# Optimization experiments

Hardware: AMD Instinct MI355X
Metric: run time of the kernel (lower is better)

## Reference

```python
import jax, jax.numpy as jnp
import numpy as np


def setup_inputs() -> dict:
    key = jax.random.key(0)
    k0, k1, k2, k3 = jax.random.split(key, 4)
    T, H, I, E = 2048, 2048, 5632, 8
    return {
        "hidden_states": jax.random.normal(k0, (T, H), dtype=jnp.float32),
        "gate_w": jax.random.normal(k1, (E, H), dtype=jnp.float32) * 0.02,
        "w1": jax.random.normal(k2, (E, 2 * I, H), dtype=jnp.float32) * 0.02,
        "w2": jax.random.normal(k3, (E, H, I), dtype=jnp.float32) * 0.02,
        "top_k": 2,
    }


def reference(hidden_states, gate_w, w1, w2, top_k):
    # hidden_states: [T, H]; gate_w: [E, H]; w1: [E, 2I, H]; w2: [E, H, I]
    T = hidden_states.shape[0]
    E = w1.shape[0]
    router_logits = hidden_states @ gate_w.T                    # [T, E]
    probs = jax.nn.softmax(router_logits, axis=-1)
    topk_w, topk_idx = jax.lax.top_k(probs, top_k)              # [T, k]
    # renormalize=False in fused_moe: use raw softmax top-k weights.
    # Dense combine matrix C[t, e] = weight of expert e for token t (0 if unrouted).
    combine = jnp.zeros((T, E), dtype=probs.dtype)
    combine = combine.at[jnp.arange(T)[:, None], topk_idx].add(topk_w)
    out = jnp.zeros_like(hidden_states)
    for e in range(E):  # small fixed expert loop
        gate_up = hidden_states @ w1[e].T                       # [T, 2I]
        g, u = jnp.split(gate_up, 2, axis=-1)
        h = jax.nn.silu(g) * u                                  # SiluAndMul
        out = out + combine[:, e:e + 1] * (h @ w2[e].T)         # [T, H]
    return out
```

## Files before the change

### kernel.cpp

```cpp
#include <hip/hip_runtime.h>
#include <hip/hip_bf16.h>

typedef __bf16 bf16_t;
typedef __bf16 bf16x8 __attribute__((ext_vector_type(8)));
typedef float  f32x4  __attribute__((ext_vector_type(4)));

constexpr int T_ = 2048, H_ = 2048, I_ = 5632, E_ = 8, S_ = T_ * 2;

constexpr size_t OFF_HB    = 0;
constexpr size_t OFF_HOUT  = OFF_HB    + (size_t)T_ * H_ * 2;
constexpr size_t OFF_DPART = OFF_HOUT  + (size_t)S_ * I_ * 2;
constexpr size_t OFF_TOS   = OFF_DPART + (size_t)S_ * H_ * 4;
constexpr size_t OFF_SOT   = OFF_TOS   + (size_t)S_ * 4;
constexpr size_t OFF_TKI   = OFF_SOT   + (size_t)S_ * 4;
constexpr size_t OFF_TKW   = OFF_TKI   + (size_t)S_ * 4;
constexpr size_t OFF_CNT   = OFF_TKW   + (size_t)S_ * 4;
constexpr size_t OFF_OFFS  = OFF_CNT   + 64;
constexpr size_t OFF_CUR   = OFF_OFFS  + 64;

__device__ __forceinline__ void gload16(const void* g, void* l) {
  __builtin_amdgcn_global_load_lds(
      (const __attribute__((address_space(1))) void*)g,
      (__attribute__((address_space(3))) void*)l, 16, 0, 0);
}

__device__ __forceinline__ bf16x8 cvt8(f32x4 a, f32x4 b) {
  bf16x8 r;
  r[0]=(bf16_t)a[0]; r[1]=(bf16_t)a[1]; r[2]=(bf16_t)a[2]; r[3]=(bf16_t)a[3];
  r[4]=(bf16_t)b[0]; r[5]=(bf16_t)b[1]; r[6]=(bf16_t)b[2]; r[7]=(bf16_t)b[3];
  return r;
}

__global__ __launch_bounds__(256)
void router_kernel(const float* __restrict__ hs, const float* __restrict__ gw,
                   int* __restrict__ tki, float* __restrict__ tkw,
                   int* __restrict__ counts, bf16_t* __restrict__ hb)
{
  const int t = blockIdx.x;
  const int tid = threadIdx.x;
  const int lane = tid & 63, wid = tid >> 6;
  const float* hrow = hs + (size_t)t * H_;
  const int c0 = tid * 8;
  float4 h0 = *(const float4*)(hrow + c0);
  float4 h1 = *(const float4*)(hrow + c0 + 4);
  bf16x8 hv;
  hv[0]=(bf16_t)h0.x; hv[1]=(bf16_t)h0.y; hv[2]=(bf16_t)h0.z; hv[3]=(bf16_t)h0.w;
  hv[4]=(bf16_t)h1.x; hv[5]=(bf16_t)h1.y; hv[6]=(bf16_t)h1.z; hv[7]=(bf16_t)h1.w;
  *(bf16x8*)(hb + (size_t)t * H_ + c0) = hv;

  float acc[E_];
  #pragma unroll
  for (int e = 0; e < E_; ++e) {
    const float* g = gw + (size_t)e * H_ + c0;
    float4 g0 = *(const float4*)(g);
    float4 g1 = *(const float4*)(g + 4);
    acc[e] = h0.x*g0.x + h0.y*g0.y + h0.z*g0.z + h0.w*g0.w
           + h1.x*g1.x + h1.y*g1.y + h1.z*g1.z + h1.w*g1.w;
  }
  #pragma unroll
  for (int e = 0; e < E_; ++e)
    #pragma unroll
    for (int o = 32; o > 0; o >>= 1)
      acc[e] += __shfl_down(acc[e], o);
  __shared__ float red[4][E_];
  if (lane == 0)
    #pragma unroll
    for (int e = 0; e < E_; ++e) red[wid][e] = acc[e];
  __syncthreads();
  if (tid == 0) {
    float l[E_];
    #pragma unroll
    for (int e = 0; e < E_; ++e) l[e] = red[0][e] + red[1][e] + red[2][e] + red[3][e];
    float m = l[0];
    #pragma unroll
    for (int e = 1; e < E_; ++e) m = fmaxf(m, l[e]);
    float p[E_]; float s = 0.f;
    #pragma unroll
    for (int e = 0; e < E_; ++e) { p[e] = __expf(l[e] - m); s += p[e]; }
    int i1 = 0;
    #pragma unroll
    for (int e = 1; e < E_; ++e) if (l[e] > l[i1]) i1 = e;
    int i2 = (i1 == 0) ? 1 : 0;
    #pragma unroll
    for (int e = 0; e < E_; ++e) if (e != i1 && l[e] > l[i2]) i2 = e;
    tki[2*t] = i1; tki[2*t+1] = i2;
    tkw[2*t] = p[i1] / s; tkw[2*t+1] = p[i2] / s;
    atomicAdd(&counts[i1], 1);
    atomicAdd(&counts[i2], 1);
  }
}

__global__ void scan_kernel(const int* __restrict__ counts, const int* __restrict__ tki,
                            int* __restrict__ offs, int* __restrict__ cursor,
                            int* __restrict__ tos, int* __restrict__ sot)
{
  if (threadIdx.x == 0) {
    int run = 0;
    for (int e = 0; e < E_; ++e) { offs[e] = run; cursor[e] = run; run += counts[e]; }
  }
  __syncthreads();
  for (int t = threadIdx.x; t < T_; t += blockDim.x) {
    #pragma unroll
    for (int k = 0; k < 2; ++k) {
      int e = tki[2*t + k];
      int s = atomicAdd(&cursor[e], 1);
      tos[s] = t;
      sot[2*t + k] = s;
    }
  }
}

constexpr int G1_BUF = 16384 + 8192;

__global__ __launch_bounds__(512, 4)
void gemm1_kernel(const bf16_t* __restrict__ hb, const float* __restrict__ w1,
                  const int* __restrict__ tos, const int* __restrict__ offs,
                  const int* __restrict__ counts, bf16_t* __restrict__ hout)
{
  const int bid = blockIdx.x;
  const int e   = bid & 7;
  const int idx = bid >> 3;
  const int mt  = idx & 3;
  const int nt  = idx >> 2;

  const int cnt = counts[e];
  const int m0 = mt * 256;
  if (m0 >= cnt) return;
  const int off = offs[e];
  const int n0 = nt * 64;

  const float* Wg = w1 + (size_t)e * (2 * (size_t)I_ * H_) + (size_t)n0 * H_;

  __shared__ char smem[2 * G1_BUF];

  const int tid = threadIdx.x;
  const int lane = tid & 63, wid = tid >> 6;
  const int wm = wid >> 1, wn = wid & 1;
  const int l15 = lane & 15, l4 = lane >> 4;

  const bf16_t* agp[2]; int aoff[2];
  #pragma unroll
  for (int i = 0; i < 2; ++i) {
    int q = wid * 2 + i;
    int w = (lane & 7) ^ ((lane >> 3) & 7);
    int row = 2 * (q * 8 + (lane >> 3)) + (w >> 2);
    int slot = off + m0 + row, mx = off + cnt - 1;
    if (slot > mx) slot = mx;
    agp[i]  = hb + (size_t)tos[slot] * H_ + (w & 3) * 8;
    aoff[i] = q * 1024;
  }
  auto stageA = [&](int b, int t) {
    char* ab = smem + b * G1_BUF;
    #pragma unroll
    for (int i = 0; i < 2; ++i) gload16(agp[i] + t * 32, ab + aoff[i]);
  };

  const int bp = tid >> 3, bw = (tid & 7) ^ (bp & 7);
  const int bn = 2 * bp + (bw >> 2);
  const size_t brow = (bn < 64) ? (size_t)bn : (size_t)(I_ + bn - 64);
  const float* bsrc = Wg + brow * H_ + (bw & 3) * 8;
  f32x4 bx, by;
  auto loadB  = [&](int k0) { bx = *(const f32x4*)(bsrc + k0); by = *(const f32x4*)(bsrc + k0 + 4); };
  auto writeB = [&](int b)  { *(bf16x8*)(smem + b * G1_BUF + 16384 + tid * 16) = cvt8(bx, by); };

  f32x4 accg[4][2], accu[4][2];
  #pragma unroll
  for (int mi = 0; mi < 4; ++mi)
    #pragma unroll
    for (int ni = 0; ni < 2; ++ni) {
      accg[mi][ni] = f32x4{0.f,0.f,0.f,0.f};
      accu[mi][ni] = f32x4{0.f,0.f,0.f,0.f};
    }

  const int phys = ((((l15 & 1) << 2) | l4) ^ ((l15 >> 1) & 7)) * 16;

  auto compute = [&](int b) {
    const char* ab = smem + b * G1_BUF;
    const char* bb = ab + 16384;
    bf16x8 af[4], bgf[2], buf2[2];
    #pragma unroll
    for (int mi = 0; mi < 4; ++mi) {
      int pr = wm * 32 + mi * 8 + (l15 >> 1);
      af[mi] = *(const bf16x8*)(ab + pr * 128 + phys);
    }
    #pragma unroll
    for (int ni = 0; ni < 2; ++ni) {
      int pb = wn * 16 + ni * 8 + (l15 >> 1);
      bgf[ni]  = *(const bf16x8*)(bb + pb * 128 + phys);
      buf2[ni] = *(const bf16x8*)(bb + (pb + 32) * 128 + phys);
    }
    #pragma unroll
    for (int mi = 0; mi < 4; ++mi)
      #pragma unroll
      for (int ni = 0; ni < 2; ++ni) {
        accg[mi][ni] = __builtin_amdgcn_mfma_f32_16x16x32_bf16(af[mi], bgf[ni],  accg[mi][ni], 0, 0, 0);
        accu[mi][ni] = __builtin_amdgcn_mfma_f32_16x16x32_bf16(af[mi], buf2[ni], accu[mi][ni], 0, 0, 0);
      }
  };

  constexpr int NK = H_ / 32;
  stageA(0, 0); loadB(0); writeB(0);
  __syncthreads();
  int cur = 0;
  for (int t = 0; t < NK; ++t) {
    if (t + 1 < NK) { stageA(cur ^ 1, t + 1); loadB((t + 1) * 32); }
    compute(cur);
    if (t + 1 < NK) writeB(cur ^ 1);
    __syncthreads();
    cur ^= 1;
  }

  #pragma unroll
  for (int mi = 0; mi < 4; ++mi)
    #pragma unroll
    for (int ni = 0; ni < 2; ++ni)
      #pragma unroll
      for (int j = 0; j < 4; ++j) {
        int rel = wm*64 + mi*16 + l4*4 + j;
        if (m0 + rel < cnt) {
          int col = n0 + wn*32 + ni*16 + l15;
          float g = accg[mi][ni][j];
          float u = accu[mi][ni][j];
          float hvv = (g / (1.0f + __expf(-g))) * u;
          hout[(size_t)(off + m0 + rel) * I_ + col] = (bf16_t)hvv;
        }
      }
}

constexpr int G2_BUF = 16384 + 4096;

__global__ __launch_bounds__(512, 4)
void gemm2_kernel(const bf16_t* __restrict__ hbuf, const float* __restrict__ w2,
                  const int* __restrict__ offs, const int* __restrict__ counts,
                  float* __restrict__ dpart)
{
  const int bid = blockIdx.x;
  const int e   = bid & 7;
  const int idx = bid >> 3;
  const int mt  = idx & 3;
  const int nt  = idx >> 2;

  const int cnt = counts[e];
  const int m0 = mt * 256;
  if (m0 >= cnt) return;
  const int off = offs[e];
  const int n0 = nt * 64;
  const float* W = w2 + (size_t)e * ((size_t)H_ * I_) + (size_t)n0 * I_;

  __shared__ char smem[2 * G2_BUF];

  const int tid = threadIdx.x;
  const int lane = tid & 63, wid = tid >> 6;
  const int wm = wid >> 1, wn = wid & 1;
  const int l15 = lane & 15, l4 = lane >> 4;

  const bf16_t* agp[2]; int aoff[2];
  #pragma unroll
  for (int i = 0; i < 2; ++i) {
    int q = wid * 2 + i;
    int w = (lane & 7) ^ ((lane >> 3) & 7);
    int row = 2 * (q * 8 + (lane >> 3)) + (w >> 2);
    int slot = off + m0 + row, mx = off + cnt - 1;
    if (slot > mx) slot = mx;
    agp[i]  = hbuf + (size_t)slot * I_ + (w & 3) * 8;
    aoff[i] = q * 1024;
  }
  auto stageA = [&](int b, int t) {
    char* ab = smem + b * G2_BUF;
    #pragma unroll
    for (int i = 0; i < 2; ++i) gload16(agp[i] + t * 32, ab + aoff[i]);
  };

  const int bp = tid >> 3, bw = (tid & 7) ^ (bp & 7);
  const int bn = 2 * bp + (bw >> 2);
  const float* bsrc = W + (size_t)bn * I_ + (bw & 3) * 8;
  f32x4 bx, by;
  auto loadB  = [&](int k0) { if (tid < 256) { bx = *(const f32x4*)(bsrc + k0); by = *(const f32x4*)(bsrc + k0 + 4); } };
  auto writeB = [&](int b)  { if (tid < 256) *(bf16x8*)(smem + b * G2_BUF + 16384 + tid * 16) = cvt8(bx, by); };

  f32x4 acc[4][2];
  #pragma unroll
  for (int mi = 0; mi < 4; ++mi)
    #pragma unroll
    for (int ni = 0; ni < 2; ++ni) acc[mi][ni] = f32x4{0.f,0.f,0.f,0.f};

  const int phys = ((((l15 & 1) << 2) | l4) ^ ((l15 >> 1) & 7)) * 16;

  auto compute = [&](int b) {
    const char* ab = smem + b * G2_BUF;
    const char* bb = ab + 16384;
    bf16x8 af[4], bf[2];
    #pragma unroll
    for (int mi = 0; mi < 4; ++mi) {
      int pr = wm * 32 + mi * 8 + (l15 >> 1);
      af[mi] = *(const bf16x8*)(ab + pr * 128 + phys);
    }
    #pragma unroll
    for (int ni = 0; ni < 2; ++ni) {
      int pb = wn * 16 + ni * 8 + (l15 >> 1);
      bf[ni] = *(const bf16x8*)(bb + pb * 128 + phys);
    }
    #pragma unroll
    for (int mi = 0; mi < 4; ++mi)
      #pragma unroll
      for (int ni = 0; ni < 2; ++ni)
        acc[mi][ni] = __builtin_amdgcn_mfma_f32_16x16x32_bf16(af[mi], bf[ni], acc[mi][ni], 0, 0, 0);
  };

  constexpr int NK = I_ / 32;
  stageA(0, 0); loadB(0); writeB(0);
  __syncthreads();
  int cur = 0;
  for (int t = 0; t < NK; ++t) {
    if (t + 1 < NK) { stageA(cur ^ 1, t + 1); loadB((t + 1) * 32); }
    compute(cur);
    if (t + 1 < NK) writeB(cur ^ 1);
    __syncthreads();
    cur ^= 1;
  }

  #pragma unroll
  for (int mi = 0; mi < 4; ++mi)
    #pragma unroll
    for (int ni = 0; ni < 2; ++ni)
      #pragma unroll
      for (int j = 0; j < 4; ++j) {
        int rel = wm*64 + mi*16 + l4*4 + j;
        if (m0 + rel < cnt) {
          int col = n0 + wn*32 + ni*16 + l15;
          dpart[(size_t)(off + m0 + rel) * H_ + col] = acc[mi][ni][j];
        }
      }
}

__global__ __launch_bounds__(256)
void combine_kernel(const float* __restrict__ dpart, const int* __restrict__ sot,
                    const float* __restrict__ tkw, float* __restrict__ out)
{
  int idx = blockIdx.x * 256 + threadIdx.x;
  int t = idx >> 9;
  int c = (idx & 511) * 4;
  float wA = tkw[2*t], wB = tkw[2*t+1];
  int sA = sot[2*t], sB = sot[2*t+1];
  float4 a = *(const float4*)(dpart + (size_t)sA * H_ + c);
  float4 b = *(const float4*)(dpart + (size_t)sB * H_ + c);
  float4 o;
  o.x = wA*a.x + wB*b.x; o.y = wA*a.y + wB*b.y;
  o.z = wA*a.z + wB*b.z; o.w = wA*a.w + wB*b.w;
  *(float4*)(out + (size_t)t * H_ + c) = o;
}

extern "C" void kernel_launch(void* const* d_in, const int* in_sizes, int n_in,
                              void* d_out, int out_size, void* d_ws, size_t ws_size,
                              hipStream_t stream) {
  const float* hs = (const float*)d_in[0];
  const float* gw = (const float*)d_in[1];
  const float* w1 = (const float*)d_in[2];
  const float* w2 = (const float*)d_in[3];
  float* out = (float*)d_out;
  char* ws = (char*)d_ws;

  bf16_t* hb    = (bf16_t*)(ws + OFF_HB);
  bf16_t* hout  = (bf16_t*)(ws + OFF_HOUT);
  float*  dpart = (float*) (ws + OFF_DPART);
  int*    tos   = (int*)   (ws + OFF_TOS);
  int*    sot   = (int*)   (ws + OFF_SOT);
  int*    tki   = (int*)   (ws + OFF_TKI);
  float*  tkw   = (float*) (ws + OFF_TKW);
  int*    cnt   = (int*)   (ws + OFF_CNT);
  int*    offp  = (int*)   (ws + OFF_OFFS);
  int*    curp  = (int*)   (ws + OFF_CUR);

  hipMemsetAsync(ws + OFF_CNT, 0, 64, stream);

  router_kernel<<<T_, 256, 0, stream>>>(hs, gw, tki, tkw, cnt, hb);
  scan_kernel<<<1, 256, 0, stream>>>(cnt, tki, offp, curp, tos, sot);
  gemm1_kernel<<<4 * (2 * I_ / 128) * E_, 512, 0, stream>>>(hb, w1, tos, offp, cnt, hout);
  gemm2_kernel<<<4 * (H_ / 64) * E_, 512, 0, stream>>>(hout, w2, offp, cnt, dpart);
  combine_kernel<<<(T_ * H_ / 4) / 256, 256, 0, stream>>>(dpart, sot, tkw, out);
}
```

Measured before the change: 1.023 ms.

## Deepen B-operand register prefetch and use explicit waitcnt pipelining in MoE GEMMs

Both expert GEMM kernels now prefetch the fp32 weight (B) tiles two k-steps ahead into alternating register sets using inline-asm global loads, with manual vmcnt/lgkmcnt waits and raw s_barrier in place of __syncthreads. The aim is to hide global-load latency for the weight stream behind the MFMA work. The second GEMM splits each B row chunk across two threads, so all 512 threads load weights instead of only half, and A fragments are now read from LDS inside the MFMA loop. The hand-counted waitcnts are fragile: a wrong count or compiler reordering around the asm could produce races or stale data.

After: 1.055 ms. 3.1% more time.

```diff
diff --git a/kernel.cpp b/kernel.cpp
--- a/kernel.cpp
+++ b/kernel.cpp
@@ -2,6 +2,7 @@
 #include <hip/hip_bf16.h>
 
 typedef __bf16 bf16_t;
+typedef __bf16 bf16x4 __attribute__((ext_vector_type(4)));
 typedef __bf16 bf16x8 __attribute__((ext_vector_type(8)));
 typedef float  f32x4  __attribute__((ext_vector_type(4)));
 
@@ -24,12 +25,26 @@
       (__attribute__((address_space(3))) void*)l, 16, 0, 0);
 }
 
+__device__ __forceinline__ void gld4(f32x4& d, const float* p) {
+  asm volatile("global_load_dwordx4 %0, %1, off" : "=&v"(d) : "v"(p) : "memory");
+}
+
 __device__ __forceinline__ bf16x8 cvt8(f32x4 a, f32x4 b) {
   bf16x8 r;
   r[0]=(bf16_t)a[0]; r[1]=(bf16_t)a[1]; r[2]=(bf16_t)a[2]; r[3]=(bf16_t)a[3];
   r[4]=(bf16_t)b[0]; r[5]=(bf16_t)b[1]; r[6]=(bf16_t)b[2]; r[7]=(bf16_t)b[3];
   return r;
 }
+__device__ __forceinline__ bf16x4 cvt4v(f32x4 a) {
+  bf16x4 r; r[0]=(bf16_t)a[0]; r[1]=(bf16_t)a[1]; r[2]=(bf16_t)a[2]; r[3]=(bf16_t)a[3];
+  return r;
+}
+
+#define SBAR() do { __builtin_amdgcn_s_barrier(); __builtin_amdgcn_sched_barrier(0); } while (0)
+#define WAITV(N) do { asm volatile("s_waitcnt vmcnt(" #N ")" ::: "memory"); \
+                      __builtin_amdgcn_sched_barrier(0); } while (0)
+#define WAITVL(N) do { asm volatile("s_waitcnt vmcnt(" #N ") lgkmcnt(0)" ::: "memory"); \
+                       __builtin_amdgcn_sched_barrier(0); } while (0)
 
 __global__ __launch_bounds__(256)
 void router_kernel(const float* __restrict__ hs, const float* __restrict__ gw,
@@ -159,9 +174,8 @@
   const int bn = 2 * bp + (bw >> 2);
   const size_t brow = (bn < 64) ? (size_t)bn : (size_t)(I_ + bn - 64);
   const float* bsrc = Wg + brow * H_ + (bw & 3) * 8;
-  f32x4 bx, by;
-  auto loadB  = [&](int k0) { bx = *(const f32x4*)(bsrc + k0); by = *(const f32x4*)(bsrc + k0 + 4); };
-  auto writeB = [&](int b)  { *(bf16x8*)(smem + b * G1_BUF + 16384 + tid * 16) = cvt8(bx, by); };
+
+  f32x4 b0x, b0y, b1x, b1y;
 
   f32x4 accg[4][2], accu[4][2];
   #pragma unroll
@@ -177,12 +191,7 @@
   auto compute = [&](int b) {
     const char* ab = smem + b * G1_BUF;
     const char* bb = ab + 16384;
-    bf16x8 af[4], bgf[2], buf2[2];
-    #pragma unroll
-    for (int mi = 0; mi < 4; ++mi) {
-      int pr = wm * 32 + mi * 8 + (l15 >> 1);
-      af[mi] = *(const bf16x8*)(ab + pr * 128 + phys);
-    }
+    bf16x8 bgf[2], buf2[2];
     #pragma unroll
     for (int ni = 0; ni < 2; ++ni) {
       int pb = wn * 16 + ni * 8 + (l15 >> 1);
@@ -190,25 +199,50 @@
       buf2[ni] = *(const bf16x8*)(bb + (pb + 32) * 128 + phys);
     }
     #pragma unroll
-    for (int mi = 0; mi < 4; ++mi)
-      #pragma unroll
-      for (int ni = 0; ni < 2; ++ni) {
-        accg[mi][ni] = __builtin_amdgcn_mfma_f32_16x16x32_bf16(af[mi], bgf[ni],  accg[mi][ni], 0, 0, 0);
-        accu[mi][ni] = __builtin_amdgcn_mfma_f32_16x16x32_bf16(af[mi], buf2[ni], accu[mi][ni], 0, 0, 0);
-      }
+    for (int mi = 0; mi < 4; ++mi) {
+      int pr = wm * 32 + mi * 8 + (l15 >> 1);
+      bf16x8 af = *(const bf16x8*)(ab + pr * 128 + phys);
+      accg[mi][0] = __builtin_amdgcn_mfma_f32_16x16x32_bf16(af, bgf[0],  accg[mi][0], 0, 0, 0);
+      accg[mi][1] = __builtin_amdgcn_mfma_f32_16x16x32_bf16(af, bgf[1],  accg[mi][1], 0, 0, 0);
+      accu[mi][0] = __builtin_amdgcn_mfma_f32_16x16x32_bf16(af, buf2[0], accu[mi][0], 0, 0, 0);
+      accu[mi][1] = __builtin_amdgcn_mfma_f32_16x16x32_bf16(af, buf2[1], accu[mi][1], 0, 0, 0);
+    }
   };
 
   constexpr int NK = H_ / 32;
-  stageA(0, 0); loadB(0); writeB(0);
-  __syncthreads();
   int cur = 0;
-  for (int t = 0; t < NK; ++t) {
-    if (t + 1 < NK) { stageA(cur ^ 1, t + 1); loadB((t + 1) * 32); }
+
+  stageA(0, 0);
+  gld4(b0x, bsrc);      gld4(b0y, bsrc + 4);
+  gld4(b1x, bsrc + 32); gld4(b1y, bsrc + 36);
+  WAITV(2);
+  *(bf16x8*)(smem + 16384 + tid * 16) = cvt8(b0x, b0y);
+  asm volatile("s_waitcnt lgkmcnt(0)" ::: "memory");
+  SBAR();
+
+  auto body = [&](int t, f32x4& lx, f32x4& ly, f32x4& wx, f32x4& wy) {
+    stageA(cur ^ 1, t + 1);
+    gld4(lx, bsrc + (t + 2) * 32);
+    gld4(ly, bsrc + (t + 2) * 32 + 4);
     compute(cur);
-    if (t + 1 < NK) writeB(cur ^ 1);
-    __syncthreads();
+    WAITV(4);
+    *(bf16x8*)(smem + (cur ^ 1) * G1_BUF + 16384 + tid * 16) = cvt8(wx, wy);
+    WAITVL(2);
+    SBAR();
     cur ^= 1;
-  }
+  };
+  for (int t = 0; t < NK - 2; t += 2) {
+    body(t,     b0x, b0y, b1x, b1y);
+    body(t + 1, b1x, b1y, b0x, b0y);
+  }
+  stageA(cur ^ 1, NK - 1);
+  compute(cur);
+  WAITV(2);
+  *(bf16x8*)(smem + (cur ^ 1) * G1_BUF + 16384 + tid * 16) = cvt8(b1x, b1y);
+  WAITVL(0);
+  SBAR();
+  cur ^= 1;
+  compute(cur);
 
   #pragma unroll
   for (int mi = 0; mi < 4; ++mi)
@@ -271,12 +305,13 @@
     for (int i = 0; i < 2; ++i) gload16(agp[i] + t * 32, ab + aoff[i]);
   };
 
-  const int bp = tid >> 3, bw = (tid & 7) ^ (bp & 7);
-  const int bn = 2 * bp + (bw >> 2);
-  const float* bsrc = W + (size_t)bn * I_ + (bw & 3) * 8;
-  f32x4 bx, by;
-  auto loadB  = [&](int k0) { if (tid < 256) { bx = *(const f32x4*)(bsrc + k0); by = *(const f32x4*)(bsrc + k0 + 4); } };
-  auto writeB = [&](int b)  { if (tid < 256) *(bf16x8*)(smem + b * G2_BUF + 16384 + tid * 16) = cvt8(bx, by); };
+  const int s2 = tid >> 1, h2 = tid & 1;
+  const int p2 = s2 >> 3, w2s = (s2 & 7) ^ (p2 & 7);
+  const int bn2 = 2 * p2 + (w2s >> 2);
+  const float* bsrc = W + (size_t)bn2 * I_ + (w2s & 3) * 8 + h2 * 4;
+  const int bldsoff = 16384 + s2 * 16 + h2 * 8;
+
+  f32x4 b0, b1;
 
   f32x4 acc[4][2];
   #pragma unroll
@@ -289,35 +324,54 @@
   auto compute = [&](int b) {
     const char* ab = smem + b * G2_BUF;
     const char* bb = ab + 16384;
-    bf16x8 af[4], bf[2];
-    #pragma unroll
-    for (int mi = 0; mi < 4; ++mi) {
-      int pr = wm * 32 + mi * 8 + (l15 >> 1);
-      af[mi] = *(const bf16x8*)(ab + pr * 128 + phys);
-    }
+    bf16x8 bf[2];
     #pragma unroll
     for (int ni = 0; ni < 2; ++ni) {
       int pb = wn * 16 + ni * 8 + (l15 >> 1);
       bf[ni] = *(const bf16x8*)(bb + pb * 128 + phys);
     }
     #pragma unroll
-    for (int mi = 0; mi < 4; ++mi)
-      #pragma unroll
-      for (int ni = 0; ni < 2; ++ni)
-        acc[mi][ni] = __builtin_amdgcn_mfma_f32_16x16x32_bf16(af[mi], bf[ni], acc[mi][ni], 0, 0, 0);
+    for (int mi = 0; mi < 4; ++mi) {
+      int pr = wm * 32 + mi * 8 + (l15 >> 1);
+      bf16x8 af = *(const bf16x8*)(ab + pr * 128 + phys);
+      acc[mi][0] = __builtin_amdgcn_mfma_f32_16x16x32_bf16(af, bf[0], acc[mi][0], 0, 0, 0);
+      acc[mi][1] = __builtin_amdgcn_mfma_f32_16x16x32_bf16(af, bf[1], acc[mi][1], 0, 0, 0);
+    }
   };
 
   constexpr int NK = I_ / 32;
-  stageA(0, 0); loadB(0); writeB(0);
-  __syncthreads();
   int cur = 0;
-  for (int t = 0; t < NK; ++t) {
-    if (t + 1 < NK) { stageA(cur ^ 1, t + 1); loadB((t + 1) * 32); }
+
+  stageA(0, 0);
+  gld4(b0, bsrc);
+  gld4(b1, bsrc + 32);
+  WAITV(1);
+  *(bf16x4*)(smem + bldsoff) = cvt4v(b0);
+  asm volatile("s_waitcnt lgkmcnt(0)" ::: "memory");
+  SBAR();
+
+  auto body = [&](int t, f32x4& lx, f32x4& wx) {
+    stageA(cur ^ 1, t + 1);
+    gld4(lx, bsrc + (t + 2) * 32);
     compute(cur);
-    if (t + 1 < NK) writeB(cur ^ 1);
-    __syncthreads();
+    WAITV(3);
+    *(bf16x4*)(smem + (cur ^ 1) * G2_BUF + bldsoff) = cvt4v(wx);
+    WAITVL(1);
+    SBAR();
     cur ^= 1;
-  }
+  };
+  for (int t = 0; t < NK - 2; t += 2) {
+    body(t,     b0, b1);
+    body(t + 1, b1, b0);
+  }
+  stageA(cur ^ 1, NK - 1);
+  compute(cur);
+  WAITV(2);
+  *(bf16x4*)(smem + (cur ^ 1) * G2_BUF + bldsoff) = cvt4v(b1);
+  WAITVL(0);
+  SBAR();
+  cur ^= 1;
+  compute(cur);
 
   #pragma unroll
   for (int mi = 0; mi < 4; ++mi)
```
